# Performance work log

Measured on AMD Instinct MI355X. Metric: run time of the kernel, lower is better.

## Reference

```python
import jax, jax.numpy as jnp
import numpy as np

N_Q_HEADS = 16
N_KV_HEADS = 4
HEAD_DIM = 64
GROUPS = N_Q_HEADS // N_KV_HEADS


def apply_rope(xq, xk, cos, sin):
    # xq: [B,S,Hq,D], xk: [B,S,Hkv,D]; cos/sin: [S, D/2]
    def rot(t):
        tr = t[..., 0::2]
        ti = t[..., 1::2]
        c = cos[None, :, None, :]
        s = sin[None, :, None, :]
        out_r = tr * c - ti * s
        out_i = tr * s + ti * c
        # interleave back: [..., D/2, 2] -> [..., D]
        return jnp.stack([out_r, out_i], axis=-1).reshape(t.shape)
    return rot(xq), rot(xk)


def setup_inputs() -> dict:
    key = jax.random.key(0)
    ks = jax.random.split(key, 8)
    B, S, DIM = 2, 2048, 1024
    x = jax.random.normal(ks[0], (B, S, DIM), jnp.float32)
    # RoPE frequencies (llama-style): theta_i = 10000^(-2i/D), angles = pos * theta
    inv_freq = 1.0 / (10000.0 ** (jnp.arange(0, HEAD_DIM, 2, dtype=jnp.float32) / HEAD_DIM))
    angles = jnp.arange(S, dtype=jnp.float32)[:, None] * inv_freq[None, :]  # [S, D/2]
    freqs_cos = jnp.cos(angles)
    freqs_sin = jnp.sin(angles)
    # additive causal mask [1,1,S,S]
    neg = jnp.float32(-1e9)
    mask = jnp.where(jnp.tril(jnp.ones((S, S), bool)), 0.0, neg)[None, None]
    scale = 0.02
    wq = jax.random.normal(ks[1], (DIM, N_Q_HEADS * HEAD_DIM), jnp.float32) * scale
    wk = jax.random.normal(ks[2], (DIM, N_KV_HEADS * HEAD_DIM), jnp.float32) * scale
    wv = jax.random.normal(ks[3], (DIM, N_KV_HEADS * HEAD_DIM), jnp.float32) * scale
    wo = jax.random.normal(ks[4], (DIM, DIM), jnp.float32) * scale
    return {"x": x, "start_pos": 0, "freqs_cos": freqs_cos, "freqs_sin": freqs_sin,
            "mask": mask, "wq": wq, "wk": wk, "wv": wv, "wo": wo}


def reference(x, start_pos, freqs_cos, freqs_sin, mask, wq, wk, wv, wo):
    B, S, DIM = x.shape
    xq = (x @ wq).reshape(B, S, N_Q_HEADS, HEAD_DIM)
    xk = (x @ wk).reshape(B, S, N_KV_HEADS, HEAD_DIM)
    xv = (x @ wv).reshape(B, S, N_KV_HEADS, HEAD_DIM)
    xq, xk = apply_rope(xq, xk, freqs_cos, freqs_sin)
    # seq_len > 1: prefill path, no KV-cache read. repeat_kv: expand kv heads by GROUPS.
    keys = jnp.repeat(xk, GROUPS, axis=2)    # [B,S,Hq,D]
    values = jnp.repeat(xv, GROUPS, axis=2)
    q = xq.transpose(0, 2, 1, 3)             # [B,H,S,D]
    k = keys.transpose(0, 2, 1, 3)
    v = values.transpose(0, 2, 1, 3)
    scores = jnp.einsum('bhqd,bhkd->bhqk', q, k) / jnp.sqrt(jnp.float32(HEAD_DIM))
    scores = scores + mask
    probs = jax.nn.softmax(scores, axis=-1)
    attn = jnp.einsum('bhqk,bhkd->bhqd', probs, v)  # [B,H,S,D]
    attn = attn.transpose(0, 2, 1, 3).reshape(B, S, DIM)
    return attn @ wo
```

## Files before the change

### kernel.cpp

```cpp
#include <hip/hip_runtime.h>

typedef __bf16 bf16_t;
typedef __bf16 bf16x8 __attribute__((ext_vector_type(8)));
typedef __bf16 bf16x4 __attribute__((ext_vector_type(4)));
typedef float f32x4 __attribute__((ext_vector_type(4)));
typedef short short4v __attribute__((ext_vector_type(4)));

#if __has_builtin(__builtin_amdgcn_exp2f)
#define EXP2F __builtin_amdgcn_exp2f
#else
#define EXP2F exp2f
#endif

#define BATCH 2
#define SEQ   2048
#define DIM   1024
#define NQH   16
#define NKVH  4
#define HD    64
#define ROWS  (BATCH*SEQ)
#define QKVN  1536
#define QSCALE 0.1803368801111f

static __device__ __forceinline__ short4v as_s4(bf16x4 v) {
    union { bf16x4 b; short4v s; } u; u.b = v; return u.s;
}

static __device__ __forceinline__ void gld16(const bf16_t* g, bf16_t* l) {
    __builtin_amdgcn_global_load_lds((const __attribute__((address_space(1))) void*)g,
                                     (__attribute__((address_space(3))) void*)l,
                                     16, 0, 0);
}

__global__ __launch_bounds__(256) void cast_x_kernel(const float* __restrict__ x,
                                                     bf16_t* __restrict__ o) {
    size_t i = ((size_t)blockIdx.x * 256 + threadIdx.x) * 4;
    float4 v = *(const float4*)(x + i);
    bf16x4 r;
    r[0] = (bf16_t)v.x; r[1] = (bf16_t)v.y; r[2] = (bf16_t)v.z; r[3] = (bf16_t)v.w;
    *(bf16x4*)(o + i) = r;
}

__global__ __launch_bounds__(256) void transpose_w_all(const float* __restrict__ wq,
                                                       const float* __restrict__ wk,
                                                       const float* __restrict__ wv,
                                                       const float* __restrict__ wo,
                                                       bf16_t* __restrict__ WqkvT,
                                                       bf16_t* __restrict__ WoT) {
    int bid = blockIdx.x;
    const float* src; bf16_t* dst; int N, nt, kt2;
    if (bid < 256)      { src = wq; dst = WqkvT;                      N = 1024; int i = bid;       nt = i & 15; kt2 = i >> 4; }
    else if (bid < 320) { src = wk; dst = WqkvT + (size_t)1024*1024;  N = 256;  int i = bid - 256; nt = i & 3;  kt2 = i >> 2; }
    else if (bid < 384) { src = wv; dst = WqkvT + (size_t)1280*1024;  N = 256;  int i = bid - 320; nt = i & 3;  kt2 = i >> 2; }
    else                { src = wo; dst = WoT;                        N = 1024; int i = bid - 384; nt = i & 15; kt2 = i >> 4; }

    __shared__ float tile[64][65];
    int t = threadIdx.x;
    {
        int r = t >> 2, cb = (t & 3) * 16;
        const float* s = src + (size_t)(kt2 * 64 + r) * N + nt * 64 + cb;
#pragma unroll
        for (int j = 0; j < 16; j += 4) {
            float4 v = *(const float4*)(s + j);
            tile[r][cb + j + 0] = v.x; tile[r][cb + j + 1] = v.y;
            tile[r][cb + j + 2] = v.z; tile[r][cb + j + 3] = v.w;
        }
    }
    __syncthreads();
    {
        int n = t >> 2, kb = (t & 3) * 16;
        union { bf16_t h[16]; uint4 u[2]; } pk;
#pragma unroll
        for (int j = 0; j < 16; ++j) pk.h[j] = (bf16_t)tile[kb + j][n];
        bf16_t* d = dst + (size_t)(nt * 64 + n) * 1024 + kt2 * 64 + kb;
        ((uint4*)d)[0] = pk.u[0];
        ((uint4*)d)[1] = pk.u[1];
    }
}

__global__ __launch_bounds__(256, 2) void gemm_qkv_kernel(const bf16_t* __restrict__ A,
                                                          const bf16_t* __restrict__ Bt,
                                                          const float* __restrict__ fcos,
                                                          const float* __restrict__ fsin,
                                                          bf16_t* __restrict__ Qb,
                                                          bf16_t* __restrict__ Kb,
                                                          bf16_t* __restrict__ Vt) {
    const int K = 1024;
    __shared__ __align__(16) bf16_t As[128 * 64];
    __shared__ __align__(16) bf16_t Bs[128 * 64];
    int t = threadIdx.x;
    int w = t >> 6, L = t & 63, quad = L >> 4, l15 = L & 15;
    int wr = (w >> 1) * 64, wc = (w & 1) * 64;

    int xid = blockIdx.x;
    int sw = (xid & 7) * 48 + (xid >> 3);
    int bnb = sw % 12;
    int bm = (sw / 12) * 128, bn = bnb * 128;

    int srow = L >> 3;
    int schunk = (L & 7) ^ srow;
    const bf16_t* Ag = A  + (size_t)(bm + w * 32 + srow) * K + schunk * 8;
    const bf16_t* Bg = Bt + (size_t)(bn + w * 32 + srow) * K + schunk * 8;
    bf16_t* Al = As + w * 2048;
    bf16_t* Bl = Bs + w * 2048;

    int rs0 = quad ^ (l15 & 7);
    int rs1 = (4 + quad) ^ (l15 & 7);

    f32x4 acc[4][4] = {};

    for (int k0 = 0; k0 < K; k0 += 64) {
        __syncthreads();
#pragma unroll
        for (int c = 0; c < 4; ++c) {
            gld16(Ag + (size_t)(c * 8) * K + k0, Al + c * 512);
            gld16(Bg + (size_t)(c * 8) * K + k0, Bl + c * 512);
        }
        __syncthreads();

#pragma unroll
        for (int kk = 0; kk < 2; ++kk) {
            int rsl = kk ? rs1 : rs0;
            bf16x8 a[4], b[4];
#pragma unroll
            for (int i = 0; i < 4; ++i) {
                a[i] = ((const bf16x8*)As)[(wr + 16 * i + l15) * 8 + rsl];
                b[i] = ((const bf16x8*)Bs)[(wc + 16 * i + l15) * 8 + rsl];
            }
#pragma unroll
            for (int i = 0; i < 4; ++i)
#pragma unroll
                for (int j = 0; j < 4; ++j)
                    acc[i][j] = __builtin_amdgcn_mfma_f32_16x16x32_bf16(a[i], b[j], acc[i][j], 0, 0, 0);
        }
    }

    int region = (bnb >= 10) ? 2 : (bnb >= 8) ? 1 : 0;
#pragma unroll
    for (int i = 0; i < 4; ++i) {
        int row0 = bm + wr + 16 * i + quad * 4;
        int b = row0 >> 11, s0 = row0 & 2047;
#pragma unroll
        for (int j = 0; j < 4; ++j) {
            int col = bn + wc + 16 * j + l15;
            if (region == 2) {
                int kvh = (col >> 6) - 20, d = col & 63;
                bf16x4 o;
#pragma unroll
                for (int r = 0; r < 4; ++r) o[r] = (bf16_t)acc[i][j][r];
                *(bf16x4*)(Vt + ((size_t)((b * NKVH + kvh) * HD + d)) * SEQ + s0) = o;
            } else {
                int d = col & 63, fi = d >> 1;
                int odd = col & 1;
#pragma unroll
                for (int r = 0; r < 4; ++r) {
                    int s = s0 + r;
                    float v = acc[i][j][r];
                    float p = __shfl_xor(v, 1);
                    float c = fcos[s * 32 + fi], sn = fsin[s * 32 + fi];
                    float o = odd ? (p * sn + v * c) : (v * c - p * sn);
                    if (region == 0) {
                        int h = col >> 6;
                        Qb[((size_t)((b * NQH + h) * SEQ + s)) * HD + d] = (bf16_t)(o * QSCALE);
                    } else {
                        int kvh = (col >> 6) - 16;
                        Kb[((size_t)((b * NKVH + kvh) * SEQ + s)) * HD + d] = (bf16_t)o;
                    }
                }
            }
        }
    }
}

__global__ __launch_bounds__(256, 2) void gemm_bt_kernel(const bf16_t* __restrict__ A,
                                                         const bf16_t* __restrict__ Bt,
                                                         float* __restrict__ C) {
    const int K = 1024, N = 1024;
    __shared__ __align__(16) bf16_t As[128 * 64];
    __shared__ __align__(16) bf16_t Bs[128 * 64];
    int t = threadIdx.x;
    int w = t >> 6, L = t & 63, quad = L >> 4, l15 = L & 15;
    int wr = (w >> 1) * 64, wc = (w & 1) * 64;

    int xid = blockIdx.x;
    int sw = (xid & 7) * 32 + (xid >> 3);
    int bm = (sw >> 3) * 128, bn = (sw & 7) * 128;

    int srow = L >> 3;
    int schunk = (L & 7) ^ srow;
    const bf16_t* Ag = A  + (size_t)(bm + w * 32 + srow) * K + schunk * 8;
    const bf16_t* Bg = Bt + (size_t)(bn + w * 32 + srow) * K + schunk * 8;
    bf16_t* Al = As + w * 2048;
    bf16_t* Bl = Bs + w * 2048;

    int rs0 = quad ^ (l15 & 7);
    int rs1 = (4 + quad) ^ (l15 & 7);

    f32x4 acc[4][4] = {};

    for (int k0 = 0; k0 < K; k0 += 64) {
        __syncthreads();
#pragma unroll
        for (int c = 0; c < 4; ++c) {
            gld16(Ag + (size_t)(c * 8) * K + k0, Al + c * 512);
            gld16(Bg + (size_t)(c * 8) * K + k0, Bl + c * 512);
        }
        __syncthreads();

#pragma unroll
        for (int kk = 0; kk < 2; ++kk) {
            int rsl = kk ? rs1 : rs0;
            bf16x8 a[4], b[4];
#pragma unroll
            for (int i = 0; i < 4; ++i) {
                a[i] = ((const bf16x8*)As)[(wr + 16 * i + l15) * 8 + rsl];
                b[i] = ((const bf16x8*)Bs)[(wc + 16 * i + l15) * 8 + rsl];
            }
#pragma unroll
            for (int i = 0; i < 4; ++i)
#pragma unroll
                for (int j = 0; j < 4; ++j)
                    acc[i][j] = __builtin_amdgcn_mfma_f32_16x16x32_bf16(a[i], b[j], acc[i][j], 0, 0, 0);
        }
    }

#pragma unroll
    for (int i = 0; i < 4; ++i) {
        int row = bm + wr + 16 * i + quad * 4;
#pragma unroll
        for (int j = 0; j < 4; ++j) {
            int col = bn + wc + 16 * j + l15;
            float* cp = C + (size_t)row * N + col;
#pragma unroll
            for (int r = 0; r < 4; ++r)
                cp[(size_t)r * N] = acc[i][j][r];
        }
    }
}

__global__ __launch_bounds__(256, 2) void attn_kernel(const bf16_t* __restrict__ Qb,
                                                      const bf16_t* __restrict__ Kb,
                                                      const bf16_t* __restrict__ Vt,
                                                      bf16_t* __restrict__ Ob) {
    int id = blockIdx.x;
    int sw = (id & 7) * 64 + (id >> 3);
    int b  = sw >> 8;
    int kv = (sw >> 6) & 3;
    int h  = kv * 4 + ((sw >> 4) & 3);
    int p  = sw & 15;

    int t = threadIdx.x, w = t >> 6, lane = t & 63, quad = lane >> 4, l15 = lane & 15;

    __shared__ __align__(16) bf16_t Ks[2][64 * 64];
    __shared__ __align__(16) bf16_t Vs[2][64 * 64];

    const bf16_t* Qbase = Qb + ((size_t)(b * NQH + h)) * SEQ * HD;
    const bf16_t* Kbase = Kb + ((size_t)(b * NKVH + kv)) * SEQ * HD;
    const bf16_t* Vbase = Vt + ((size_t)(b * NKVH + kv)) * HD * SEQ;

    int so = t >> 3, sc = t & 7, ssw = (sc ^ (so & 7)) * 8;
    const bf16_t* kS0 = Kbase + (size_t)so * HD + ssw;
    const bf16_t* vS0 = Vbase + (size_t)so * SEQ + ssw;
    int ldso = w * 512;

#pragma unroll 1
    for (int ph = 0; ph < 2; ++ph) {
        int qt = ph ? (31 - p) : p;
        int Q0 = qt * 64;
        int wq = Q0 + 16 * w + l15;
        int ktmax = qt;

        bf16x8 aq[2];
#pragma unroll
        for (int ks = 0; ks < 2; ++ks)
            aq[ks] = *(const bf16x8*)(Qbase + (size_t)wq * HD + ks * 32 + quad * 8);

        f32x4 acc_o[4] = {};
        float rs = 0.f;

        __syncthreads();
        gld16(kS0,                 Ks[0] + ldso);
        gld16(kS0 + 32 * HD,       Ks[0] + ldso + 2048);
        gld16(vS0,                 Vs[0] + ldso);
        gld16(vS0 + (size_t)32 * SEQ, Vs[0] + ldso + 2048);

        int cur = 0;
        for (int kt = 0; kt <= ktmax; ++kt) {
            __syncthreads();
            if (kt < ktmax) {
                const bf16_t* kp = kS0 + (size_t)(kt + 1) * 64 * HD;
                const bf16_t* vp = vS0 + (size_t)(kt + 1) * 64;
                bf16_t* kd = Ks[cur ^ 1] + ldso;
                bf16_t* vd = Vs[cur ^ 1] + ldso;
                gld16(kp,                 kd);
                gld16(kp + 32 * HD,       kd + 2048);
                gld16(vp,                 vd);
                gld16(vp + (size_t)32 * SEQ, vd + 2048);
            }
            const bf16_t* KsC = Ks[cur];
            const bf16_t* VsC = Vs[cur];

            short4v bp[4];
            if (kt == ktmax) {
                int kb = kt * 64 + quad * 4;
#pragma unroll
                for (int x = 0; x < 4; ++x) {
                    int key = 16 * x + l15;
                    bf16x8 ak0 = ((const bf16x8*)KsC)[key * 8 + ((0 + quad) ^ (key & 7))];
                    bf16x8 ak1 = ((const bf16x8*)KsC)[key * 8 + ((4 + quad) ^ (key & 7))];
                    f32x4 z = {0.f, 0.f, 0.f, 0.f};
                    z = __builtin_amdgcn_mfma_f32_16x16x32_bf16(ak0, aq[0], z, 0, 0, 0);
                    z = __builtin_amdgcn_mfma_f32_16x16x32_bf16(ak1, aq[1], z, 0, 0, 0);
                    bf16x4 pb;
#pragma unroll
                    for (int r = 0; r < 4; ++r) {
                        float pv = (kb + 16 * x + r <= wq) ? EXP2F(z[r]) : 0.f;
                        rs += pv; pb[r] = (bf16_t)pv;
                    }
                    bp[x] = as_s4(pb);
                }
            } else {
#pragma unroll
                for (int x = 0; x < 4; ++x) {
                    int key = 16 * x + l15;
                    bf16x8 ak0 = ((const bf16x8*)KsC)[key * 8 + ((0 + quad) ^ (key & 7))];
                    bf16x8 ak1 = ((const bf16x8*)KsC)[key * 8 + ((4 + quad) ^ (key & 7))];
                    f32x4 z = {0.f, 0.f, 0.f, 0.f};
                    z = __builtin_amdgcn_mfma_f32_16x16x32_bf16(ak0, aq[0], z, 0, 0, 0);
                    z = __builtin_amdgcn_mfma_f32_16x16x32_bf16(ak1, aq[1], z, 0, 0, 0);
                    bf16x4 pb;
#pragma unroll
                    for (int r = 0; r < 4; ++r) {
                        float pv = EXP2F(z[r]);
                        rs += pv; pb[r] = (bf16_t)pv;
                    }
                    bp[x] = as_s4(pb);
                }
            }

            __builtin_amdgcn_s_setprio(1);
#pragma unroll
            for (int dt = 0; dt < 4; ++dt) {
                int d = 16 * dt + l15;
#pragma unroll
                for (int x = 0; x < 4; ++x) {
                    int pos = (2 * x + (quad >> 1)) ^ (d & 7);
                    bf16x4 av = *(const bf16x4*)(VsC + d * 64 + pos * 8 + (quad & 1) * 4);
                    acc_o[dt] = __builtin_amdgcn_mfma_f32_16x16x16bf16_1k(as_s4(av), bp[x], acc_o[dt], 0, 0, 0);
                }
            }
            __builtin_amdgcn_s_setprio(0);
            cur ^= 1;
        }

        rs += __shfl_xor(rs, 16);
        rs += __shfl_xor(rs, 32);
        float rinv = 1.0f / rs;
        bf16_t* obase = Ob + (size_t)(b * SEQ + wq) * DIM + h * HD;
#pragma unroll
        for (int dt = 0; dt < 4; ++dt) {
            bf16x4 o;
#pragma unroll
            for (int r = 0; r < 4; ++r) o[r] = (bf16_t)(acc_o[dt][r] * rinv);
            *(bf16x4*)(obase + 16 * dt + quad * 4) = o;
        }
    }
}

extern "C" void kernel_launch(void* const* d_in, const int* in_sizes, int n_in,
                              void* d_out, int out_size, void* d_ws, size_t ws_size,
                              hipStream_t stream) {
    const float* x    = (const float*)d_in[0];
    const float* fcos = (const float*)d_in[2];
    const float* fsin = (const float*)d_in[3];
    const float* wq   = (const float*)d_in[5];
    const float* wk   = (const float*)d_in[6];
    const float* wv   = (const float*)d_in[7];
    const float* wo   = (const float*)d_in[8];
    float* out = (float*)d_out;

    char* ws = (char*)d_ws;
    bf16_t* Xb    = (bf16_t*)(ws + 0);
    bf16_t* Attnb = Xb;
    bf16_t* WqkvT = (bf16_t*)(ws + 8388608);
    bf16_t* WoT   = (bf16_t*)(ws + 11534336);
    bf16_t* Qb    = (bf16_t*)(ws + 13631488);
    bf16_t* Kb    = (bf16_t*)(ws + 22020096);
    bf16_t* Vt    = (bf16_t*)(ws + 24117248);

    cast_x_kernel<<<ROWS * DIM / 1024, 256, 0, stream>>>(x, Xb);
    transpose_w_all<<<640, 256, 0, stream>>>(wq, wk, wv, wo, WqkvT, WoT);

    gemm_qkv_kernel<<<QKVN / 128 * (ROWS / 128), 256, 0, stream>>>(Xb, WqkvT, fcos, fsin, Qb, Kb, Vt);

    attn_kernel<<<512, 256, 0, stream>>>(Qb, Kb, Vt, Attnb);

    gemm_bt_kernel<<<(DIM / 128) * (ROWS / 128), 256, 0, stream>>>(Attnb, WoT, out);
}
```

Measured before the change: 180.2 us.

## Shrink GEMM M-tiles to 64 and fuse paired causal query tiles in attention

```diff
diff --git a/kernel.cpp b/kernel.cpp
--- a/kernel.cpp
+++ b/kernel.cpp
@@ -78,7 +78,7 @@
     }
 }
 
-__global__ __launch_bounds__(256, 2) void gemm_qkv_kernel(const bf16_t* __restrict__ A,
+__global__ __launch_bounds__(256, 3) void gemm_qkv_kernel(const bf16_t* __restrict__ A,
                                                           const bf16_t* __restrict__ Bt,
                                                           const float* __restrict__ fcos,
                                                           const float* __restrict__ fsin,
@@ -86,49 +86,50 @@
                                                           bf16_t* __restrict__ Kb,
                                                           bf16_t* __restrict__ Vt) {
     const int K = 1024;
-    __shared__ __align__(16) bf16_t As[128 * 64];
+    __shared__ __align__(16) bf16_t As[64 * 64];
     __shared__ __align__(16) bf16_t Bs[128 * 64];
     int t = threadIdx.x;
     int w = t >> 6, L = t & 63, quad = L >> 4, l15 = L & 15;
-    int wr = (w >> 1) * 64, wc = (w & 1) * 64;
+    int wr = (w >> 1) * 32, wc = (w & 1) * 64;
 
     int xid = blockIdx.x;
-    int sw = (xid & 7) * 48 + (xid >> 3);
+    int sw = (xid & 7) * 96 + (xid >> 3);
     int bnb = sw % 12;
-    int bm = (sw / 12) * 128, bn = bnb * 128;
+    int bm = (sw / 12) * 64, bn = bnb * 128;
 
     int srow = L >> 3;
     int schunk = (L & 7) ^ srow;
-    const bf16_t* Ag = A  + (size_t)(bm + w * 32 + srow) * K + schunk * 8;
+    const bf16_t* Ag = A  + (size_t)(bm + w * 16 + srow) * K + schunk * 8;
     const bf16_t* Bg = Bt + (size_t)(bn + w * 32 + srow) * K + schunk * 8;
-    bf16_t* Al = As + w * 2048;
+    bf16_t* Al = As + w * 1024;
     bf16_t* Bl = Bs + w * 2048;
 
     int rs0 = quad ^ (l15 & 7);
     int rs1 = (4 + quad) ^ (l15 & 7);
 
-    f32x4 acc[4][4] = {};
+    f32x4 acc[2][4] = {};
 
     for (int k0 = 0; k0 < K; k0 += 64) {
         __syncthreads();
-#pragma unroll
-        for (int c = 0; c < 4; ++c) {
-            gld16(Ag + (size_t)(c * 8) * K + k0, Al + c * 512);
+        gld16(Ag + k0,                 Al);
+        gld16(Ag + (size_t)8 * K + k0, Al + 512);
+#pragma unroll
+        for (int c = 0; c < 4; ++c)
             gld16(Bg + (size_t)(c * 8) * K + k0, Bl + c * 512);
-        }
         __syncthreads();
 
 #pragma unroll
         for (int kk = 0; kk < 2; ++kk) {
             int rsl = kk ? rs1 : rs0;
-            bf16x8 a[4], b[4];
-#pragma unroll
-            for (int i = 0; i < 4; ++i) {
+            bf16x8 a[2], b[4];
+#pragma unroll
+            for (int i = 0; i < 2; ++i)
                 a[i] = ((const bf16x8*)As)[(wr + 16 * i + l15) * 8 + rsl];
-                b[i] = ((const bf16x8*)Bs)[(wc + 16 * i + l15) * 8 + rsl];
-            }
-#pragma unroll
-            for (int i = 0; i < 4; ++i)
+#pragma unroll
+            for (int j = 0; j < 4; ++j)
+                b[j] = ((const bf16x8*)Bs)[(wc + 16 * j + l15) * 8 + rsl];
+#pragma unroll
+            for (int i = 0; i < 2; ++i)
 #pragma unroll
                 for (int j = 0; j < 4; ++j)
                     acc[i][j] = __builtin_amdgcn_mfma_f32_16x16x32_bf16(a[i], b[j], acc[i][j], 0, 0, 0);
@@ -137,7 +138,7 @@
 
     int region = (bnb >= 10) ? 2 : (bnb >= 8) ? 1 : 0;
 #pragma unroll
-    for (int i = 0; i < 4; ++i) {
+    for (int i = 0; i < 2; ++i) {
         int row0 = bm + wr + 16 * i + quad * 4;
         int b = row0 >> 11, s0 = row0 & 2047;
 #pragma unroll
@@ -176,48 +177,49 @@
                                                          const bf16_t* __restrict__ Bt,
                                                          float* __restrict__ C) {
     const int K = 1024, N = 1024;
-    __shared__ __align__(16) bf16_t As[128 * 64];
+    __shared__ __align__(16) bf16_t As[64 * 64];
     __shared__ __align__(16) bf16_t Bs[128 * 64];
     int t = threadIdx.x;
     int w = t >> 6, L = t & 63, quad = L >> 4, l15 = L & 15;
-    int wr = (w >> 1) * 64, wc = (w & 1) * 64;
+    int wr = (w >> 1) * 32, wc = (w & 1) * 64;
 
     int xid = blockIdx.x;
-    int sw = (xid & 7) * 32 + (xid >> 3);
-    int bm = (sw >> 3) * 128, bn = (sw & 7) * 128;
+    int sw = (xid & 7) * 64 + (xid >> 3);
+    int bm = (sw >> 3) * 64, bn = (sw & 7) * 128;
 
     int srow = L >> 3;
     int schunk = (L & 7) ^ srow;
-    const bf16_t* Ag = A  + (size_t)(bm + w * 32 + srow) * K + schunk * 8;
+    const bf16_t* Ag = A  + (size_t)(bm + w * 16 + srow) * K + schunk * 8;
     const bf16_t* Bg = Bt + (size_t)(bn + w * 32 + srow) * K + schunk * 8;
-    bf16_t* Al = As + w * 2048;
+    bf16_t* Al = As + w * 1024;
     bf16_t* Bl = Bs + w * 2048;
 
     int rs0 = quad ^ (l15 & 7);
     int rs1 = (4 + quad) ^ (l15 & 7);
 
-    f32x4 acc[4][4] = {};
+    f32x4 acc[2][4] = {};
 
     for (int k0 = 0; k0 < K; k0 += 64) {
         __syncthreads();
-#pragma unroll
-        for (int c = 0; c < 4; ++c) {
-            gld16(Ag + (size_t)(c * 8) * K + k0, Al + c * 512);
+        gld16(Ag + k0,                 Al);
+        gld16(Ag + (size_t)8 * K + k0, Al + 512);
+#pragma unroll
+        for (int c = 0; c < 4; ++c)
             gld16(Bg + (size_t)(c * 8) * K + k0, Bl + c * 512);
-        }
         __syncthreads();
 
 #pragma unroll
         for (int kk = 0; kk < 2; ++kk) {
             int rsl = kk ? rs1 : rs0;
-            bf16x8 a[4], b[4];
-#pragma unroll
-            for (int i = 0; i < 4; ++i) {
+            bf16x8 a[2], b[4];
+#pragma unroll
+            for (int i = 0; i < 2; ++i)
                 a[i] = ((const bf16x8*)As)[(wr + 16 * i + l15) * 8 + rsl];
-                b[i] = ((const bf16x8*)Bs)[(wc + 16 * i + l15) * 8 + rsl];
-            }
-#pragma unroll
-            for (int i = 0; i < 4; ++i)
+#pragma unroll
+            for (int j = 0; j < 4; ++j)
+                b[j] = ((const bf16x8*)Bs)[(wc + 16 * j + l15) * 8 + rsl];
+#pragma unroll
+            for (int i = 0; i < 2; ++i)
 #pragma unroll
                 for (int j = 0; j < 4; ++j)
                     acc[i][j] = __builtin_amdgcn_mfma_f32_16x16x32_bf16(a[i], b[j], acc[i][j], 0, 0, 0);
@@ -225,7 +227,7 @@
     }
 
 #pragma unroll
-    for (int i = 0; i < 4; ++i) {
+    for (int i = 0; i < 2; ++i) {
         int row = bm + wr + 16 * i + quad * 4;
 #pragma unroll
         for (int j = 0; j < 4; ++j) {
@@ -263,107 +265,125 @@
     const bf16_t* vS0 = Vbase + (size_t)so * SEQ + ssw;
     int ldso = w * 512;
 
-#pragma unroll 1
-    for (int ph = 0; ph < 2; ++ph) {
-        int qt = ph ? (31 - p) : p;
-        int Q0 = qt * 64;
-        int wq = Q0 + 16 * w + l15;
-        int ktmax = qt;
-
-        bf16x8 aq[2];
-#pragma unroll
-        for (int ks = 0; ks < 2; ++ks)
-            aq[ks] = *(const bf16x8*)(Qbase + (size_t)wq * HD + ks * 32 + quad * 8);
-
-        f32x4 acc_o[4] = {};
-        float rs = 0.f;
-
+    int ktB = 31 - p;
+    int wqA = p * 64 + 16 * w + l15;
+    int wqB = ktB * 64 + 16 * w + l15;
+
+    bf16x8 aqA[2], aqB[2];
+#pragma unroll
+    for (int ks = 0; ks < 2; ++ks) {
+        aqA[ks] = *(const bf16x8*)(Qbase + (size_t)wqA * HD + ks * 32 + quad * 8);
+        aqB[ks] = *(const bf16x8*)(Qbase + (size_t)wqB * HD + ks * 32 + quad * 8);
+    }
+
+    f32x4 accA[4] = {}, accB[4] = {};
+    float rsA = 0.f, rsB = 0.f;
+
+    gld16(kS0,                    Ks[0] + ldso);
+    gld16(kS0 + 32 * HD,          Ks[0] + ldso + 2048);
+    gld16(vS0,                    Vs[0] + ldso);
+    gld16(vS0 + (size_t)32 * SEQ, Vs[0] + ldso + 2048);
+
+    int cur = 0;
+    for (int kt = 0; kt <= ktB; ++kt) {
         __syncthreads();
-        gld16(kS0,                 Ks[0] + ldso);
-        gld16(kS0 + 32 * HD,       Ks[0] + ldso + 2048);
-        gld16(vS0,                 Vs[0] + ldso);
-        gld16(vS0 + (size_t)32 * SEQ, Vs[0] + ldso + 2048);
-
-        int cur = 0;
-        for (int kt = 0; kt <= ktmax; ++kt) {
-            __syncthreads();
-            if (kt < ktmax) {
-                const bf16_t* kp = kS0 + (size_t)(kt + 1) * 64 * HD;
-                const bf16_t* vp = vS0 + (size_t)(kt + 1) * 64;
-                bf16_t* kd = Ks[cur ^ 1] + ldso;
-                bf16_t* vd = Vs[cur ^ 1] + ldso;
-                gld16(kp,                 kd);
-                gld16(kp + 32 * HD,       kd + 2048);
-                gld16(vp,                 vd);
-                gld16(vp + (size_t)32 * SEQ, vd + 2048);
-            }
-            const bf16_t* KsC = Ks[cur];
-            const bf16_t* VsC = Vs[cur];
-
-            short4v bp[4];
-            if (kt == ktmax) {
-                int kb = kt * 64 + quad * 4;
-#pragma unroll
-                for (int x = 0; x < 4; ++x) {
-                    int key = 16 * x + l15;
-                    bf16x8 ak0 = ((const bf16x8*)KsC)[key * 8 + ((0 + quad) ^ (key & 7))];
-                    bf16x8 ak1 = ((const bf16x8*)KsC)[key * 8 + ((4 + quad) ^ (key & 7))];
-                    f32x4 z = {0.f, 0.f, 0.f, 0.f};
-                    z = __builtin_amdgcn_mfma_f32_16x16x32_bf16(ak0, aq[0], z, 0, 0, 0);
-                    z = __builtin_amdgcn_mfma_f32_16x16x32_bf16(ak1, aq[1], z, 0, 0, 0);
-                    bf16x4 pb;
+        if (kt < ktB) {
+            const bf16_t* kp = kS0 + (size_t)(kt + 1) * 64 * HD;
+            const bf16_t* vp = vS0 + (size_t)(kt + 1) * 64;
+            bf16_t* kd = Ks[cur ^ 1] + ldso;
+            bf16_t* vd = Vs[cur ^ 1] + ldso;
+            gld16(kp,                    kd);
+            gld16(kp + 32 * HD,          kd + 2048);
+            gld16(vp,                    vd);
+            gld16(vp + (size_t)32 * SEQ, vd + 2048);
+        }
+        const bf16_t* KsC = Ks[cur];
+        const bf16_t* VsC = Vs[cur];
+        bool actA = (kt <= p);
+
+        short4v bpA[4], bpB[4];
+        int kb = kt * 64 + quad * 4;
+#pragma unroll
+        for (int x = 0; x < 4; ++x) {
+            int key = 16 * x + l15;
+            bf16x8 ak0 = ((const bf16x8*)KsC)[key * 8 + ((0 + quad) ^ (key & 7))];
+            bf16x8 ak1 = ((const bf16x8*)KsC)[key * 8 + ((4 + quad) ^ (key & 7))];
+            {
+                f32x4 z = {0.f, 0.f, 0.f, 0.f};
+                z = __builtin_amdgcn_mfma_f32_16x16x32_bf16(ak0, aqB[0], z, 0, 0, 0);
+                z = __builtin_amdgcn_mfma_f32_16x16x32_bf16(ak1, aqB[1], z, 0, 0, 0);
+                bf16x4 pb;
+                if (kt == ktB) {
 #pragma unroll
                     for (int r = 0; r < 4; ++r) {
-                        float pv = (kb + 16 * x + r <= wq) ? EXP2F(z[r]) : 0.f;
-                        rs += pv; pb[r] = (bf16_t)pv;
+                        float pv = (kb + 16 * x + r <= wqB) ? EXP2F(z[r]) : 0.f;
+                        rsB += pv; pb[r] = (bf16_t)pv;
                     }
-                    bp[x] = as_s4(pb);
-                }
-            } else {
-#pragma unroll
-                for (int x = 0; x < 4; ++x) {
-                    int key = 16 * x + l15;
-                    bf16x8 ak0 = ((const bf16x8*)KsC)[key * 8 + ((0 + quad) ^ (key & 7))];
-                    bf16x8 ak1 = ((const bf16x8*)KsC)[key * 8 + ((4 + quad) ^ (key & 7))];
-                    f32x4 z = {0.f, 0.f, 0.f, 0.f};
-                    z = __builtin_amdgcn_mfma_f32_16x16x32_bf16(ak0, aq[0], z, 0, 0, 0);
-                    z = __builtin_amdgcn_mfma_f32_16x16x32_bf16(ak1, aq[1], z, 0, 0, 0);
-                    bf16x4 pb;
+                } else {
 #pragma unroll
                     for (int r = 0; r < 4; ++r) {
                         float pv = EXP2F(z[r]);
-                        rs += pv; pb[r] = (bf16_t)pv;
+                        rsB += pv; pb[r] = (bf16_t)pv;
                     }
-                    bp[x] = as_s4(pb);
                 }
+                bpB[x] = as_s4(pb);
             }
-
-            __builtin_amdgcn_s_setprio(1);
-#pragma unroll
-            for (int dt = 0; dt < 4; ++dt) {
-                int d = 16 * dt + l15;
-#pragma unroll
-                for (int x = 0; x < 4; ++x) {
-                    int pos = (2 * x + (quad >> 1)) ^ (d & 7);
-                    bf16x4 av = *(const bf16x4*)(VsC + d * 64 + pos * 8 + (quad & 1) * 4);
-                    acc_o[dt] = __builtin_amdgcn_mfma_f32_16x16x16bf16_1k(as_s4(av), bp[x], acc_o[dt], 0, 0, 0);
+            if (actA) {
+                f32x4 z = {0.f, 0.f, 0.f, 0.f};
+                z = __builtin_amdgcn_mfma_f32_16x16x32_bf16(ak0, aqA[0], z, 0, 0, 0);
+                z = __builtin_amdgcn_mfma_f32_16x16x32_bf16(ak1, aqA[1], z, 0, 0, 0);
+                bf16x4 pb;
+                if (kt == p) {
+#pragma unroll
+                    for (int r = 0; r < 4; ++r) {
+                        float pv = (kb + 16 * x + r <= wqA) ? EXP2F(z[r]) : 0.f;
+                        rsA += pv; pb[r] = (bf16_t)pv;
+                    }
+                } else {
+#pragma unroll
+                    for (int r = 0; r < 4; ++r) {
+                        float pv = EXP2F(z[r]);
+                        rsA += pv; pb[r] = (bf16_t)pv;
+                    }
                 }
+                bpA[x] = as_s4(pb);
             }
-            __builtin_amdgcn_s_setprio(0);
-            cur ^= 1;
-        }
-
-        rs += __shfl_xor(rs, 16);
-        rs += __shfl_xor(rs, 32);
-        float rinv = 1.0f / rs;
-        bf16_t* obase = Ob + (size_t)(b * SEQ + wq) * DIM + h * HD;
+        }
+
+        __builtin_amdgcn_s_setprio(1);
 #pragma unroll
         for (int dt = 0; dt < 4; ++dt) {
-            bf16x4 o;
-#pragma unroll
-            for (int r = 0; r < 4; ++r) o[r] = (bf16_t)(acc_o[dt][r] * rinv);
-            *(bf16x4*)(obase + 16 * dt + quad * 4) = o;
-        }
+            int d = 16 * dt + l15;
+#pragma unroll
+            for (int x = 0; x < 4; ++x) {
+                int pos = (2 * x + (quad >> 1)) ^ (d & 7);
+                bf16x4 av = *(const bf16x4*)(VsC + d * 64 + pos * 8 + (quad & 1) * 4);
+                accB[dt] = __builtin_amdgcn_mfma_f32_16x16x16bf16_1k(as_s4(av), bpB[x], accB[dt], 0, 0, 0);
+                if (actA)
+                    accA[dt] = __builtin_amdgcn_mfma_f32_16x16x16bf16_1k(as_s4(av), bpA[x], accA[dt], 0, 0, 0);
+            }
+        }
+        __builtin_amdgcn_s_setprio(0);
+        cur ^= 1;
+    }
+
+    rsA += __shfl_xor(rsA, 16);
+    rsA += __shfl_xor(rsA, 32);
+    rsB += __shfl_xor(rsB, 16);
+    rsB += __shfl_xor(rsB, 32);
+    float riA = 1.0f / rsA, riB = 1.0f / rsB;
+    bf16_t* obA = Ob + (size_t)(b * SEQ + wqA) * DIM + h * HD;
+    bf16_t* obB = Ob + (size_t)(b * SEQ + wqB) * DIM + h * HD;
+#pragma unroll
+    for (int dt = 0; dt < 4; ++dt) {
+        bf16x4 oA, oB;
+#pragma unroll
+        for (int r = 0; r < 4; ++r) {
+            oA[r] = (bf16_t)(accA[dt][r] * riA);
+            oB[r] = (bf16_t)(accB[dt][r] * riB);
+        }
+        *(bf16x4*)(obA + 16 * dt + quad * 4) = oA;
+        *(bf16x4*)(obB + 16 * dt + quad * 4) = oB;
     }
 }
 
@@ -391,9 +411,9 @@
     cast_x_kernel<<<ROWS * DIM / 1024, 256, 0, stream>>>(x, Xb);
     transpose_w_all<<<640, 256, 0, stream>>>(wq, wk, wv, wo, WqkvT, WoT);
 
-    gemm_qkv_kernel<<<QKVN / 128 * (ROWS / 128), 256, 0, stream>>>(Xb, WqkvT, fcos, fsin, Qb, Kb, Vt);
+    gemm_qkv_kernel<<<(QKVN / 128) * (ROWS / 64), 256, 0, stream>>>(Xb, WqkvT, fcos, fsin, Qb, Kb, Vt);
 
     attn_kernel<<<512, 256, 0, stream>>>(Qb, Kb, Vt, Attnb);
 
-    gemm_bt_kernel<<<(DIM / 128) * (ROWS / 128), 256, 0, stream>>>(Attnb, WoT, out);
-}
+    gemm_bt_kernel<<<(DIM / 128) * (ROWS / 64), 256, 0, stream>>>(Attnb, WoT, out);
+}
```

After: 184.3 us. 1.02x slower.

## Halve GEMM M-tiles for more blocks and double attention key tile to 128

Applied to the files above, without the earlier changes.

```diff
diff --git a/kernel.cpp b/kernel.cpp
--- a/kernel.cpp
+++ b/kernel.cpp
@@ -78,7 +78,7 @@
     }
 }
 
-__global__ __launch_bounds__(256, 2) void gemm_qkv_kernel(const bf16_t* __restrict__ A,
+__global__ __launch_bounds__(256, 3) void gemm_qkv_kernel(const bf16_t* __restrict__ A,
                                                           const bf16_t* __restrict__ Bt,
                                                           const float* __restrict__ fcos,
                                                           const float* __restrict__ fsin,
@@ -86,49 +86,50 @@
                                                           bf16_t* __restrict__ Kb,
                                                           bf16_t* __restrict__ Vt) {
     const int K = 1024;
-    __shared__ __align__(16) bf16_t As[128 * 64];
+    __shared__ __align__(16) bf16_t As[64 * 64];
     __shared__ __align__(16) bf16_t Bs[128 * 64];
     int t = threadIdx.x;
     int w = t >> 6, L = t & 63, quad = L >> 4, l15 = L & 15;
-    int wr = (w >> 1) * 64, wc = (w & 1) * 64;
+    int wr = (w >> 1) * 32, wc = (w & 1) * 64;
 
     int xid = blockIdx.x;
-    int sw = (xid & 7) * 48 + (xid >> 3);
+    int sw = (xid & 7) * 96 + (xid >> 3);
     int bnb = sw % 12;
-    int bm = (sw / 12) * 128, bn = bnb * 128;
+    int bm = (sw / 12) * 64, bn = bnb * 128;
 
     int srow = L >> 3;
     int schunk = (L & 7) ^ srow;
-    const bf16_t* Ag = A  + (size_t)(bm + w * 32 + srow) * K + schunk * 8;
+    const bf16_t* Ag = A  + (size_t)(bm + w * 16 + srow) * K + schunk * 8;
     const bf16_t* Bg = Bt + (size_t)(bn + w * 32 + srow) * K + schunk * 8;
-    bf16_t* Al = As + w * 2048;
+    bf16_t* Al = As + w * 1024;
     bf16_t* Bl = Bs + w * 2048;
 
     int rs0 = quad ^ (l15 & 7);
     int rs1 = (4 + quad) ^ (l15 & 7);
 
-    f32x4 acc[4][4] = {};
+    f32x4 acc[2][4] = {};
 
     for (int k0 = 0; k0 < K; k0 += 64) {
         __syncthreads();
-#pragma unroll
-        for (int c = 0; c < 4; ++c) {
-            gld16(Ag + (size_t)(c * 8) * K + k0, Al + c * 512);
+        gld16(Ag + k0,                 Al);
+        gld16(Ag + (size_t)8 * K + k0, Al + 512);
+#pragma unroll
+        for (int c = 0; c < 4; ++c)
             gld16(Bg + (size_t)(c * 8) * K + k0, Bl + c * 512);
-        }
         __syncthreads();
 
 #pragma unroll
         for (int kk = 0; kk < 2; ++kk) {
             int rsl = kk ? rs1 : rs0;
-            bf16x8 a[4], b[4];
-#pragma unroll
-            for (int i = 0; i < 4; ++i) {
+            bf16x8 a[2], b[4];
+#pragma unroll
+            for (int i = 0; i < 2; ++i)
                 a[i] = ((const bf16x8*)As)[(wr + 16 * i + l15) * 8 + rsl];
-                b[i] = ((const bf16x8*)Bs)[(wc + 16 * i + l15) * 8 + rsl];
-            }
-#pragma unroll
-            for (int i = 0; i < 4; ++i)
+#pragma unroll
+            for (int j = 0; j < 4; ++j)
+                b[j] = ((const bf16x8*)Bs)[(wc + 16 * j + l15) * 8 + rsl];
+#pragma unroll
+            for (int i = 0; i < 2; ++i)
 #pragma unroll
                 for (int j = 0; j < 4; ++j)
                     acc[i][j] = __builtin_amdgcn_mfma_f32_16x16x32_bf16(a[i], b[j], acc[i][j], 0, 0, 0);
@@ -137,7 +138,7 @@
 
     int region = (bnb >= 10) ? 2 : (bnb >= 8) ? 1 : 0;
 #pragma unroll
-    for (int i = 0; i < 4; ++i) {
+    for (int i = 0; i < 2; ++i) {
         int row0 = bm + wr + 16 * i + quad * 4;
         int b = row0 >> 11, s0 = row0 & 2047;
 #pragma unroll
@@ -176,48 +177,49 @@
                                                          const bf16_t* __restrict__ Bt,
                                                          float* __restrict__ C) {
     const int K = 1024, N = 1024;
-    __shared__ __align__(16) bf16_t As[128 * 64];
+    __shared__ __align__(16) bf16_t As[64 * 64];
     __shared__ __align__(16) bf16_t Bs[128 * 64];
     int t = threadIdx.x;
     int w = t >> 6, L = t & 63, quad = L >> 4, l15 = L & 15;
-    int wr = (w >> 1) * 64, wc = (w & 1) * 64;
+    int wr = (w >> 1) * 32, wc = (w & 1) * 64;
 
     int xid = blockIdx.x;
-    int sw = (xid & 7) * 32 + (xid >> 3);
-    int bm = (sw >> 3) * 128, bn = (sw & 7) * 128;
+    int sw = (xid & 7) * 64 + (xid >> 3);
+    int bm = (sw >> 3) * 64, bn = (sw & 7) * 128;
 
     int srow = L >> 3;
     int schunk = (L & 7) ^ srow;
-    const bf16_t* Ag = A  + (size_t)(bm + w * 32 + srow) * K + schunk * 8;
+    const bf16_t* Ag = A  + (size_t)(bm + w * 16 + srow) * K + schunk * 8;
     const bf16_t* Bg = Bt + (size_t)(bn + w * 32 + srow) * K + schunk * 8;
-    bf16_t* Al = As + w * 2048;
+    bf16_t* Al = As + w * 1024;
     bf16_t* Bl = Bs + w * 2048;
 
     int rs0 = quad ^ (l15 & 7);
     int rs1 = (4 + quad) ^ (l15 & 7);
 
-    f32x4 acc[4][4] = {};
+    f32x4 acc[2][4] = {};
 
     for (int k0 = 0; k0 < K; k0 += 64) {
         __syncthreads();
-#pragma unroll
-        for (int c = 0; c < 4; ++c) {
-            gld16(Ag + (size_t)(c * 8) * K + k0, Al + c * 512);
+        gld16(Ag + k0,                 Al);
+        gld16(Ag + (size_t)8 * K + k0, Al + 512);
+#pragma unroll
+        for (int c = 0; c < 4; ++c)
             gld16(Bg + (size_t)(c * 8) * K + k0, Bl + c * 512);
-        }
         __syncthreads();
 
 #pragma unroll
         for (int kk = 0; kk < 2; ++kk) {
             int rsl = kk ? rs1 : rs0;
-            bf16x8 a[4], b[4];
-#pragma unroll
-            for (int i = 0; i < 4; ++i) {
+            bf16x8 a[2], b[4];
+#pragma unroll
+            for (int i = 0; i < 2; ++i)
                 a[i] = ((const bf16x8*)As)[(wr + 16 * i + l15) * 8 + rsl];
-                b[i] = ((const bf16x8*)Bs)[(wc + 16 * i + l15) * 8 + rsl];
-            }
-#pragma unroll
-            for (int i = 0; i < 4; ++i)
+#pragma unroll
+            for (int j = 0; j < 4; ++j)
+                b[j] = ((const bf16x8*)Bs)[(wc + 16 * j + l15) * 8 + rsl];
+#pragma unroll
+            for (int i = 0; i < 2; ++i)
 #pragma unroll
                 for (int j = 0; j < 4; ++j)
                     acc[i][j] = __builtin_amdgcn_mfma_f32_16x16x32_bf16(a[i], b[j], acc[i][j], 0, 0, 0);
@@ -225,7 +227,7 @@
     }
 
 #pragma unroll
-    for (int i = 0; i < 4; ++i) {
+    for (int i = 0; i < 2; ++i) {
         int row = bm + wr + 16 * i + quad * 4;
 #pragma unroll
         for (int j = 0; j < 4; ++j) {
@@ -251,24 +253,22 @@
 
     int t = threadIdx.x, w = t >> 6, lane = t & 63, quad = lane >> 4, l15 = lane & 15;
 
-    __shared__ __align__(16) bf16_t Ks[2][64 * 64];
-    __shared__ __align__(16) bf16_t Vs[2][64 * 64];
+    __shared__ __align__(16) bf16_t Ks[2][128 * 64];
+    __shared__ __align__(16) bf16_t Vs[2][64 * 128];
 
     const bf16_t* Qbase = Qb + ((size_t)(b * NQH + h)) * SEQ * HD;
     const bf16_t* Kbase = Kb + ((size_t)(b * NKVH + kv)) * SEQ * HD;
     const bf16_t* Vbase = Vt + ((size_t)(b * NKVH + kv)) * HD * SEQ;
 
-    int so = t >> 3, sc = t & 7, ssw = (sc ^ (so & 7)) * 8;
-    const bf16_t* kS0 = Kbase + (size_t)so * HD + ssw;
-    const bf16_t* vS0 = Vbase + (size_t)so * SEQ + ssw;
+    const bf16_t* kS0 = Kbase + (size_t)(t >> 3) * HD + (size_t)(((t & 7) ^ ((t >> 3) & 7)) * 8);
+    const bf16_t* vS0 = Vbase + (size_t)(t >> 4) * SEQ + (size_t)(((t & 15) ^ ((t >> 4) & 7)) * 8);
     int ldso = w * 512;
 
 #pragma unroll 1
     for (int ph = 0; ph < 2; ++ph) {
         int qt = ph ? (31 - p) : p;
-        int Q0 = qt * 64;
-        int wq = Q0 + 16 * w + l15;
-        int ktmax = qt;
+        int wq = qt * 64 + 16 * w + l15;
+        int ktmax = qt >> 1;
 
         bf16x8 aq[2];
 #pragma unroll
@@ -279,32 +279,34 @@
         float rs = 0.f;
 
         __syncthreads();
-        gld16(kS0,                 Ks[0] + ldso);
-        gld16(kS0 + 32 * HD,       Ks[0] + ldso + 2048);
-        gld16(vS0,                 Vs[0] + ldso);
-        gld16(vS0 + (size_t)32 * SEQ, Vs[0] + ldso + 2048);
+#pragma unroll
+        for (int j = 0; j < 4; ++j) {
+            gld16(kS0 + (size_t)j * 32 * HD, Ks[0] + ldso + j * 2048);
+            gld16(vS0 + (size_t)j * 16 * SEQ, Vs[0] + ldso + j * 2048);
+        }
 
         int cur = 0;
         for (int kt = 0; kt <= ktmax; ++kt) {
             __syncthreads();
             if (kt < ktmax) {
-                const bf16_t* kp = kS0 + (size_t)(kt + 1) * 64 * HD;
-                const bf16_t* vp = vS0 + (size_t)(kt + 1) * 64;
+                const bf16_t* kp = kS0 + (size_t)(kt + 1) * 128 * HD;
+                const bf16_t* vp = vS0 + (size_t)(kt + 1) * 128;
                 bf16_t* kd = Ks[cur ^ 1] + ldso;
                 bf16_t* vd = Vs[cur ^ 1] + ldso;
-                gld16(kp,                 kd);
-                gld16(kp + 32 * HD,       kd + 2048);
-                gld16(vp,                 vd);
-                gld16(vp + (size_t)32 * SEQ, vd + 2048);
+#pragma unroll
+                for (int j = 0; j < 4; ++j) {
+                    gld16(kp + (size_t)j * 32 * HD, kd + j * 2048);
+                    gld16(vp + (size_t)j * 16 * SEQ, vd + j * 2048);
+                }
             }
             const bf16_t* KsC = Ks[cur];
             const bf16_t* VsC = Vs[cur];
 
-            short4v bp[4];
+            short4v bp[8];
             if (kt == ktmax) {
-                int kb = kt * 64 + quad * 4;
-#pragma unroll
-                for (int x = 0; x < 4; ++x) {
+                int kb = kt * 128 + quad * 4;
+#pragma unroll
+                for (int x = 0; x < 8; ++x) {
                     int key = 16 * x + l15;
                     bf16x8 ak0 = ((const bf16x8*)KsC)[key * 8 + ((0 + quad) ^ (key & 7))];
                     bf16x8 ak1 = ((const bf16x8*)KsC)[key * 8 + ((4 + quad) ^ (key & 7))];
@@ -321,7 +323,7 @@
                 }
             } else {
 #pragma unroll
-                for (int x = 0; x < 4; ++x) {
+                for (int x = 0; x < 8; ++x) {
                     int key = 16 * x + l15;
                     bf16x8 ak0 = ((const bf16x8*)KsC)[key * 8 + ((0 + quad) ^ (key & 7))];
                     bf16x8 ak1 = ((const bf16x8*)KsC)[key * 8 + ((4 + quad) ^ (key & 7))];
@@ -343,9 +345,9 @@
             for (int dt = 0; dt < 4; ++dt) {
                 int d = 16 * dt + l15;
 #pragma unroll
-                for (int x = 0; x < 4; ++x) {
+                for (int x = 0; x < 8; ++x) {
                     int pos = (2 * x + (quad >> 1)) ^ (d & 7);
-                    bf16x4 av = *(const bf16x4*)(VsC + d * 64 + pos * 8 + (quad & 1) * 4);
+                    bf16x4 av = *(const bf16x4*)(VsC + d * 128 + pos * 8 + (quad & 1) * 4);
                     acc_o[dt] = __builtin_amdgcn_mfma_f32_16x16x16bf16_1k(as_s4(av), bp[x], acc_o[dt], 0, 0, 0);
                 }
             }
@@ -391,9 +393,9 @@
     cast_x_kernel<<<ROWS * DIM / 1024, 256, 0, stream>>>(x, Xb);
     transpose_w_all<<<640, 256, 0, stream>>>(wq, wk, wv, wo, WqkvT, WoT);
 
-    gemm_qkv_kernel<<<QKVN / 128 * (ROWS / 128), 256, 0, stream>>>(Xb, WqkvT, fcos, fsin, Qb, Kb, Vt);
+    gemm_qkv_kernel<<<(QKVN / 128) * (ROWS / 64), 256, 0, stream>>>(Xb, WqkvT, fcos, fsin, Qb, Kb, Vt);
 
     attn_kernel<<<512, 256, 0, stream>>>(Qb, Kb, Vt, Attnb);
 
-    gemm_bt_kernel<<<(DIM / 128) * (ROWS / 128), 256, 0, stream>>>(Attnb, WoT, out);
-}
+    gemm_bt_kernel<<<(DIM / 128) * (ROWS / 64), 256, 0, stream>>>(Attnb, WoT, out);
+}
```

After: 167.3 us. 1.08x faster.
